# Performance work log

Measured on AMD Instinct MI355X. Metric: run time of the kernel, lower is better.

## Reference

```python
import itertools
import jax, jax.numpy as jnp
import numpy as np

N_BLOCKS = 2_097_152  # number of 8x8 blocks; 512 MB fp32 input


def _make_alpha():
    a = np.array([1.0 / np.sqrt(2)] + [1.0] * 7)
    return jnp.asarray(np.outer(a, a), dtype=jnp.float32)  # [8,8]


def _make_dct_tensor():
    t = np.zeros((8, 8, 8, 8), dtype=np.float32)
    for x, y, u, v in itertools.product(range(8), repeat=4):
        t[x, y, u, v] = np.cos((2 * u + 1) * x * np.pi / 16) * np.cos((2 * v + 1) * y * np.pi / 16)
    return jnp.asarray(t)  # [8,8,8,8]


def setup_inputs() -> dict:
    key = jax.random.key(0)
    image = jax.random.normal(key, (N_BLOCKS, 8, 8), dtype=jnp.float32)
    return {"image": image, "alpha": _make_alpha(), "dct_tensor": _make_dct_tensor()}


def reference(image, alpha, dct_tensor):
    # result[n,u,v] = 0.25 * sum_{x,y} (image[n,x,y] * alpha[x,y]) * T[x,y,u,v] + 128
    scaled = image * alpha  # broadcast over batch of 8x8 blocks
    out = 0.25 * jnp.einsum("nxy,xyuv->nuv", scaled, dct_tensor) + 128.0
    return out
```

## Files before the change

kernel.cpp:

```cpp
#include <hip/hip_runtime.h>


#define WG      256
#define BPW     (WG / 8)
#define STRIDE4 17

__global__ __launch_bounds__(WG, 8) void dct8x8_kernel(
    const float* __restrict__ image,
    const float* __restrict__ alpha,
    const float* __restrict__ dct,
    float* __restrict__ out,
    int nblocks)
{
    __shared__ float4 lds4[BPW * STRIDE4];

    const int t = threadIdx.x;
    const int b = t >> 3;
    const int r = t & 7;

    float M[8][8];
#pragma unroll
    for (int i = 0; i < 8; ++i) {
        const float ai = 0.5f * alpha[i * 8 + 1];
#pragma unroll
        for (int j = 0; j < 8; ++j)
            M[i][j] = ai * dct[i * 512 + j * 8];
    }

    float mu[8];
#pragma unroll
    for (int x = 0; x < 8; ++x)
        mu[x] = 0.5f * alpha[x * 8 + 1] * dct[x * 512 + r * 8];

    const long long gblk = (long long)blockIdx.x * BPW + b;
    const bool valid = gblk < (long long)nblocks;
    const size_t base4 = (size_t)gblk * 16 + (size_t)r * 2;

    float row[8];
    if (valid) {
        const float4 lo = ((const float4*)image)[base4 + 0];
        const float4 hi = ((const float4*)image)[base4 + 1];
        row[0] = lo.x; row[1] = lo.y; row[2] = lo.z; row[3] = lo.w;
        row[4] = hi.x; row[5] = hi.y; row[6] = hi.z; row[7] = hi.w;
    } else {
#pragma unroll
        for (int j = 0; j < 8; ++j) row[j] = 0.0f;
    }

    float P[8];
#pragma unroll
    for (int v = 0; v < 8; ++v) {
        float s = 0.0f;
#pragma unroll
        for (int y = 0; y < 8; ++y)
            s = fmaf(row[y], M[y][v], s);
        P[v] = s;
    }

    lds4[b * STRIDE4 + r * 2 + 0] = make_float4(P[0], P[1], P[2], P[3]);
    lds4[b * STRIDE4 + r * 2 + 1] = make_float4(P[4], P[5], P[6], P[7]);
    __syncthreads();

    float O[8] = {128.0f, 128.0f, 128.0f, 128.0f, 128.0f, 128.0f, 128.0f, 128.0f};
#pragma unroll
    for (int x = 0; x < 8; ++x) {
        const float4 plo = lds4[b * STRIDE4 + x * 2 + 0];
        const float4 phi = lds4[b * STRIDE4 + x * 2 + 1];
        const float m = mu[x];
        O[0] = fmaf(m, plo.x, O[0]);
        O[1] = fmaf(m, plo.y, O[1]);
        O[2] = fmaf(m, plo.z, O[2]);
        O[3] = fmaf(m, plo.w, O[3]);
        O[4] = fmaf(m, phi.x, O[4]);
        O[5] = fmaf(m, phi.y, O[5]);
        O[6] = fmaf(m, phi.z, O[6]);
        O[7] = fmaf(m, phi.w, O[7]);
    }

    if (valid) {
        ((float4*)out)[base4 + 0] = make_float4(O[0], O[1], O[2], O[3]);
        ((float4*)out)[base4 + 1] = make_float4(O[4], O[5], O[6], O[7]);
    }
}

extern "C" void kernel_launch(void* const* d_in, const int* in_sizes, int n_in,
                              void* d_out, int out_size, void* d_ws, size_t ws_size,
                              hipStream_t stream) {
    const float* image = (const float*)d_in[0];
    const float* alpha = (const float*)d_in[1];
    const float* dct   = (const float*)d_in[2];
    float* outp = (float*)d_out;

    const int nblocks = in_sizes[0] / 64;
    const long long wgs = ((long long)nblocks + BPW - 1) / BPW;

    dct8x8_kernel<<<(int)wgs, WG, 0, stream>>>(image, alpha, dct, outp, nblocks);
}
```

Before: 220.3 us.

## Use persistent grid-stride loop with register prefetch and nontemporal stores

Replaces the one-tile-per-workgroup launch with a persistent grid of at most 2048 workgroups that loop over tiles. Each iteration prefetches the next tile's rows into registers, and the LDS buffer is double-buffered so only one barrier per tile is needed. The 64 coefficient loads per thread become one load per lane broadcast with readlane. Output is written with nontemporal stores. The aim is to hide global load latency and cut per-workgroup setup cost for this bandwidth-bound 512 MB stream. In exchange, the capped grid may reduce memory-level parallelism, and register pressure rises from the prefetch and the 64 broadcast values.

```diff
diff --git a/kernel.cpp b/kernel.cpp
--- a/kernel.cpp
+++ b/kernel.cpp
@@ -4,6 +4,9 @@
 #define WG      256
 #define BPW     (WG / 8)
 #define STRIDE4 17
+#define MAXWG   2048
+
+typedef float fx4 __attribute__((ext_vector_type(4)));
 
 __global__ __launch_bounds__(WG, 8) void dct8x8_kernel(
     const float* __restrict__ image,
@@ -12,74 +15,96 @@
     float* __restrict__ out,
     int nblocks)
 {
-    __shared__ float4 lds4[BPW * STRIDE4];
+    __shared__ float4 lds4[2 * BPW * STRIDE4];
 
     const int t = threadIdx.x;
     const int b = t >> 3;
     const int r = t & 7;
+    const int lane = t & 63;
 
-    float M[8][8];
+    float mv;
+    {
+        const int i = lane >> 3, j = lane & 7;
+        mv = 0.5f * alpha[i * 8 + 1] * dct[i * 512 + j * 8];
+    }
+    float M[64];
 #pragma unroll
-    for (int i = 0; i < 8; ++i) {
-        const float ai = 0.5f * alpha[i * 8 + 1];
-#pragma unroll
-        for (int j = 0; j < 8; ++j)
-            M[i][j] = ai * dct[i * 512 + j * 8];
-    }
+    for (int k = 0; k < 64; ++k)
+        M[k] = __int_as_float(__builtin_amdgcn_readlane(__float_as_int(mv), k));
 
     float mu[8];
 #pragma unroll
     for (int x = 0; x < 8; ++x)
         mu[x] = 0.5f * alpha[x * 8 + 1] * dct[x * 512 + r * 8];
 
-    const long long gblk = (long long)blockIdx.x * BPW + b;
-    const bool valid = gblk < (long long)nblocks;
-    const size_t base4 = (size_t)gblk * 16 + (size_t)r * 2;
+    const long long ntiles = ((long long)nblocks + BPW - 1) / BPW;
+    const float4* __restrict__ in4 = (const float4*)image;
+    fx4* __restrict__ o4 = (fx4*)out;
 
-    float row[8];
-    if (valid) {
-        const float4 lo = ((const float4*)image)[base4 + 0];
-        const float4 hi = ((const float4*)image)[base4 + 1];
-        row[0] = lo.x; row[1] = lo.y; row[2] = lo.z; row[3] = lo.w;
-        row[4] = hi.x; row[5] = hi.y; row[6] = hi.z; row[7] = hi.w;
-    } else {
-#pragma unroll
-        for (int j = 0; j < 8; ++j) row[j] = 0.0f;
+    long long tile = blockIdx.x;
+    if (tile >= ntiles) return;
+
+    float4 clo = make_float4(0.f, 0.f, 0.f, 0.f), chi = clo;
+    if (tile * BPW + b < nblocks) {
+        const size_t p = (size_t)tile * (BPW * 16) + 2 * t;
+        clo = in4[p]; chi = in4[p + 1];
     }
 
-    float P[8];
+    int bufsel = 0;
+    while (tile < ntiles) {
+        const long long nxt = tile + gridDim.x;
+        float4 nlo = make_float4(0.f, 0.f, 0.f, 0.f), nhi = nlo;
+        if (nxt < ntiles && nxt * BPW + b < nblocks) {
+            const size_t p = (size_t)nxt * (BPW * 16) + 2 * t;
+            nlo = in4[p]; nhi = in4[p + 1];
+        }
+
+        float P[8];
+        {
+            const float row[8] = {clo.x, clo.y, clo.z, clo.w,
+                                  chi.x, chi.y, chi.z, chi.w};
 #pragma unroll
-    for (int v = 0; v < 8; ++v) {
-        float s = 0.0f;
+            for (int v = 0; v < 8; ++v) {
+                float s = 0.0f;
 #pragma unroll
-        for (int y = 0; y < 8; ++y)
-            s = fmaf(row[y], M[y][v], s);
-        P[v] = s;
-    }
+                for (int y = 0; y < 8; ++y)
+                    s = fmaf(row[y], M[y * 8 + v], s);
+                P[v] = s;
+            }
+        }
 
-    lds4[b * STRIDE4 + r * 2 + 0] = make_float4(P[0], P[1], P[2], P[3]);
-    lds4[b * STRIDE4 + r * 2 + 1] = make_float4(P[4], P[5], P[6], P[7]);
-    __syncthreads();
+        float4* buf = &lds4[bufsel * (BPW * STRIDE4)];
+        buf[b * STRIDE4 + r * 2 + 0] = make_float4(P[0], P[1], P[2], P[3]);
+        buf[b * STRIDE4 + r * 2 + 1] = make_float4(P[4], P[5], P[6], P[7]);
+        __syncthreads();
 
-    float O[8] = {128.0f, 128.0f, 128.0f, 128.0f, 128.0f, 128.0f, 128.0f, 128.0f};
+        float O[8] = {128.f, 128.f, 128.f, 128.f, 128.f, 128.f, 128.f, 128.f};
 #pragma unroll
-    for (int x = 0; x < 8; ++x) {
-        const float4 plo = lds4[b * STRIDE4 + x * 2 + 0];
-        const float4 phi = lds4[b * STRIDE4 + x * 2 + 1];
-        const float m = mu[x];
-        O[0] = fmaf(m, plo.x, O[0]);
-        O[1] = fmaf(m, plo.y, O[1]);
-        O[2] = fmaf(m, plo.z, O[2]);
-        O[3] = fmaf(m, plo.w, O[3]);
-        O[4] = fmaf(m, phi.x, O[4]);
-        O[5] = fmaf(m, phi.y, O[5]);
-        O[6] = fmaf(m, phi.z, O[6]);
-        O[7] = fmaf(m, phi.w, O[7]);
-    }
+        for (int x = 0; x < 8; ++x) {
+            const float4 plo = buf[b * STRIDE4 + x * 2 + 0];
+            const float4 phi = buf[b * STRIDE4 + x * 2 + 1];
+            const float m = mu[x];
+            O[0] = fmaf(m, plo.x, O[0]);
+            O[1] = fmaf(m, plo.y, O[1]);
+            O[2] = fmaf(m, plo.z, O[2]);
+            O[3] = fmaf(m, plo.w, O[3]);
+            O[4] = fmaf(m, phi.x, O[4]);
+            O[5] = fmaf(m, phi.y, O[5]);
+            O[6] = fmaf(m, phi.z, O[6]);
+            O[7] = fmaf(m, phi.w, O[7]);
+        }
 
-    if (valid) {
-        ((float4*)out)[base4 + 0] = make_float4(O[0], O[1], O[2], O[3]);
-        ((float4*)out)[base4 + 1] = make_float4(O[4], O[5], O[6], O[7]);
+        if (tile * BPW + b < nblocks) {
+            const size_t p = (size_t)tile * (BPW * 16) + 2 * t;
+            fx4 v0 = {O[0], O[1], O[2], O[3]};
+            fx4 v1 = {O[4], O[5], O[6], O[7]};
+            __builtin_nontemporal_store(v0, &o4[p]);
+            __builtin_nontemporal_store(v1, &o4[p + 1]);
+        }
+
+        clo = nlo; chi = nhi;
+        tile = nxt;
+        bufsel ^= 1;
     }
 }
 
@@ -92,7 +117,9 @@
     float* outp = (float*)d_out;
 
     const int nblocks = in_sizes[0] / 64;
-    const long long wgs = ((long long)nblocks + BPW - 1) / BPW;
+    const long long ntiles = ((long long)nblocks + BPW - 1) / BPW;
+    int grid = (int)((ntiles < MAXWG) ? ntiles : MAXWG);
+    if (grid < 1) grid = 1;
 
-    dct8x8_kernel<<<(int)wgs, WG, 0, stream>>>(image, alpha, dct, outp, nblocks);
+    dct8x8_kernel<<<grid, WG, 0, stream>>>(image, alpha, dct, outp, nblocks);
 }
```

After: 478.3 us. 117% more time.
